# Optimization experiments

Hardware: AMD Instinct MI355X
Metric: run time of the kernel (lower is better)

## Reference

```python
import jax, jax.numpy as jnp
import numpy as np
import math

D_MODEL = 1024
N_HEADS = 16
RANK = 16
SCALE = 16.0
T_LEN = 2048
BSZ = 2


def setup_inputs() -> dict:
    key = jax.random.key(0)
    ks = jax.random.split(key, 12)
    d, r = D_MODEL, RANK
    inp = {
        "query": jax.random.normal(ks[0], (T_LEN, BSZ, d), dtype=jnp.float32),
        "key": jax.random.normal(ks[1], (T_LEN, BSZ, d), dtype=jnp.float32),
        "value": jax.random.normal(ks[2], (T_LEN, BSZ, d), dtype=jnp.float32),
        "need_weights": 0,
        "attn_mask": 0,
        "in_proj_weight": jax.random.normal(ks[3], (3 * d, d), dtype=jnp.float32) * 0.02,
        "in_proj_bias": jax.random.normal(ks[4], (3 * d,), dtype=jnp.float32) * 0.02,
        "out_w": jax.random.normal(ks[5], (d, d), dtype=jnp.float32) * 0.02,
        "out_b": jax.random.normal(ks[6], (d,), dtype=jnp.float32) * 0.02,
        "k_a": jax.random.normal(ks[7], (r, d), dtype=jnp.float32) * 0.02,
        "k_b": jax.random.normal(ks[8], (r, d), dtype=jnp.float32) * 0.02,
        "v_a": jax.random.normal(ks[9], (r, d), dtype=jnp.float32) * 0.02,
        "v_b": jax.random.normal(ks[10], (r, d), dtype=jnp.float32) * 0.02,
    }
    return inp


def reference(query, key, value, need_weights, attn_mask,
              in_proj_weight, in_proj_bias, out_w, out_b,
              k_a, k_b, v_a, v_b):
    # NOTE: original module computes q,k,v all from `query` (self-attention);
    # `key`, `value`, `need_weights`, `attn_mask` are unused in the math.
    T, B, d = query.shape
    H = N_HEADS
    hd = d // H
    qkv = query @ in_proj_weight.T + in_proj_bias  # (T, B, 3d)
    q, k, v = jnp.split(qkv, 3, axis=-1)
    s = SCALE / RANK
    # LoRA low-rank updates on K and V (computed from query)
    k = k + s * ((query @ k_a.T) @ k_b)
    v = v + s * ((query @ v_a.T) @ v_b)
    # split heads: (T, B, H, hd)
    qh = q.reshape(T, B, H, hd)
    kh = k.reshape(T, B, H, hd)
    vh = v.reshape(T, B, H, hd)
    scale = 1.0 / math.sqrt(hd)
    scores = jnp.einsum('tbhd,sbhd->bhts', qh * scale, kh)  # (B, H, T, T)
    attn = jax.nn.softmax(scores, axis=-1)
    out = jnp.einsum('bhts,sbhd->tbhd', attn, vh).reshape(T, B, d)
    out = out @ out_w.T + out_b
    return out
```

## Files before the change

kernel.cpp:

```cpp
#include <hip/hip_runtime.h>
#include <stdint.h>

#define DEVI __device__ __forceinline__

typedef unsigned short u16;
typedef __attribute__((ext_vector_type(4))) float f32x4;
typedef __attribute__((ext_vector_type(16))) float f32x16;
typedef __attribute__((ext_vector_type(8))) short bf16x8;
typedef __attribute__((ext_vector_type(2))) unsigned int u32x2;

constexpr int T_LEN = 2048;
constexpr int BSZ   = 2;
constexpr int DM    = 1024;
constexpr int NH    = 16;
constexpr int HD    = 64;
constexpr int MROWS = T_LEN * BSZ;
constexpr float LORA_S = 16.0f / 16.0f;
constexpr float QSCALE = 0.125f * 1.4426950408889634f;

DEVI u16 f2bf(float x) {
  union { float f; uint32_t u; } v; v.f = x;
  uint32_t r = (v.u + 0x7FFFu + ((v.u >> 16) & 1u)) >> 16;
  return (u16)r;
}

DEVI uint32_t pk2bf(float a, float b) {
  return (uint32_t)f2bf(a) | ((uint32_t)f2bf(b) << 16);
}

DEVI uint32_t e2r(float x) {
  union { float f; uint32_t u; } v;
  v.f = __builtin_amdgcn_exp2f(x);
  return v.u;
}

DEVI void gload_lds16(const void* g, void* l) {
  __builtin_amdgcn_global_load_lds(
      (const __attribute__((address_space(1))) void*)g,
      (__attribute__((address_space(3))) void*)l, 16, 0, 0);
}

DEVI f32x4 mfma16(bf16x8 a, bf16x8 b, f32x4 c) {
  return __builtin_amdgcn_mfma_f32_16x16x32_bf16(a, b, c, 0, 0, 0);
}
DEVI f32x16 mfma32(bf16x8 a, bf16x8 b, f32x16 c) {
  return __builtin_amdgcn_mfma_f32_32x32x16_bf16(a, b, c, 0, 0, 0);
}

DEVI int kvswz(int rc, int l) { return rc * 128 + ((l ^ (rc & 15)) << 3); }

#define WAITBAR(N)                                        \
  do {                                                    \
    asm volatile("s_waitcnt vmcnt(" #N ")" ::: "memory"); \
    __builtin_amdgcn_sched_barrier(0);                    \
    __builtin_amdgcn_s_barrier();                         \
    __builtin_amdgcn_sched_barrier(0);                    \
  } while (0)

#define BARO()                                            \
  do {                                                    \
    __builtin_amdgcn_sched_barrier(0);                    \
    __builtin_amdgcn_s_barrier();                         \
    __builtin_amdgcn_sched_barrier(0);                    \
  } while (0)

__global__ void prep_kernel(const float* __restrict__ query,
                            const float* __restrict__ W,
                            const float* __restrict__ ka, const float* __restrict__ kb,
                            const float* __restrict__ va, const float* __restrict__ vb,
                            const float* __restrict__ ow,
                            u16* __restrict__ Wm, u16* __restrict__ Wo,
                            u16* __restrict__ Aq) {
  const int W3 = 3 * DM * DM;
  const int WO = DM * DM;
  const int AQ = MROWS * DM;
  const int total = W3 + WO + AQ;
  for (int idx = blockIdx.x * blockDim.x + threadIdx.x; idx < total;
       idx += gridDim.x * blockDim.x) {
    if (idx < W3) {
      const int n = idx >> 10, k = idx & 1023;
      float w = W[idx];
      if (n >= 2 * DM) {
        const int n2 = n - 2 * DM;
        float a = 0.f;
#pragma unroll
        for (int r = 0; r < 16; ++r) a += va[r * DM + k] * vb[r * DM + n2];
        w += LORA_S * a;
      } else if (n >= DM) {
        const int n2 = n - DM;
        float a = 0.f;
#pragma unroll
        for (int r = 0; r < 16; ++r) a += ka[r * DM + k] * kb[r * DM + n2];
        w += LORA_S * a;
      }
      Wm[idx] = f2bf(w);
    } else if (idx < W3 + WO) {
      const int i = idx - W3;
      Wo[i] = f2bf(ow[i]);
    } else {
      const int i = idx - W3 - WO;
      Aq[i] = f2bf(query[i]);
    }
  }
}

template <int EPIL>
__global__ __launch_bounds__(256, 4) void gemm_bt(
    const u16* __restrict__ A, const u16* __restrict__ Bt,
    const float* __restrict__ bias, float* __restrict__ Cf,
    u16* __restrict__ Qb, u16* __restrict__ Kb, u16* __restrict__ Vt,
    int M, int N, int K) {
  constexpr int BM = 128, BN = 128, BK = 32;
  __shared__ alignas(16) u16 SM[2][2][4096];
  const int tid = threadIdx.x;
  const int wv = tid >> 6, ln = tid & 63;
  const int l16 = ln & 15, lhi = ln >> 4;

  const int bid = blockIdx.x;
  const int half = (N >> 7) >> 1;
  const int x = bid & 7, j = bid >> 3;
  const int rq = x >> 1, ch = x & 1;
  const int jc = j % half, jr = j / half;
  const int row0 = (rq * 8 + jr) * BM;
  const int col0 = (ch * half + jc) * BN;
  const int wr = (wv >> 1) * 64, wc = (wv & 1) * 64;

  f32x4 acc[4][4];
#pragma unroll
  for (int i = 0; i < 4; ++i)
#pragma unroll
    for (int j2 = 0; j2 < 4; ++j2) acc[i][j2] = f32x4{0.f, 0.f, 0.f, 0.f};

  const int lrA = wv * 16 + (ln >> 3);
  const int lrB = lrA + 8;
  const int s_ = ln & 7;
  const int la = s_ ^ (lrA & 7), lb = s_ ^ (lrB & 7);
  const int ra = lrA + 64 * (la >> 2), ca = (la & 3) * 8;
  const int rb = lrB + 64 * (lb >> 2), cb = (lb & 3) * 8;

  const u16* pa0 = A + (size_t)(row0 + ra) * K + ca;
  const u16* pa1 = A + (size_t)(row0 + rb) * K + cb;
  const u16* pb0 = Bt + (size_t)(col0 + ra) * K + ca;
  const u16* pb1 = Bt + (size_t)(col0 + rb) * K + cb;

  auto stagep = [&](int buf) {
    gload_lds16(pa0, &SM[buf][0][(wv * 16) * 64]);
    gload_lds16(pa1, &SM[buf][0][(wv * 16 + 8) * 64]);
    gload_lds16(pb0, &SM[buf][1][(wv * 16) * 64]);
    gload_lds16(pb1, &SM[buf][1][(wv * 16 + 8) * 64]);
    pa0 += BK; pa1 += BK; pb0 += BK; pb1 += BK;
  };

  auto compute = [&](int buf) {
    const u16* Al = SM[buf][0];
    const u16* Bl = SM[buf][1];
    bf16x8 af[4], bfr[4];
#pragma unroll
    for (int m = 0; m < 4; ++m) {
      const int r = wr + m * 16 + l16, lr = r & 63;
      const int sl = (lhi | ((r >> 6) << 2)) ^ (lr & 7);
      af[m] = *(const bf16x8*)&Al[lr * 64 + sl * 8];
    }
#pragma unroll
    for (int n = 0; n < 4; ++n) {
      const int r = wc + n * 16 + l16, lr = r & 63;
      const int sl = (lhi | ((r >> 6) << 2)) ^ (lr & 7);
      bfr[n] = *(const bf16x8*)&Bl[lr * 64 + sl * 8];
    }
#pragma unroll
    for (int m = 0; m < 4; ++m)
#pragma unroll
      for (int n = 0; n < 4; ++n) acc[m][n] = mfma16(af[m], bfr[n], acc[m][n]);
  };

  const int NS = K / BK;
  stagep(0); stagep(1);

  for (int t = 0; t < NS - 2; t += 2) {
    WAITBAR(4); compute(0); BARO(); stagep(0);
    WAITBAR(4); compute(1); BARO(); stagep(1);
  }
  WAITBAR(4); compute(0);
  WAITBAR(0); compute(1);

  if constexpr (EPIL == 0) {
    if (col0 >= 2 * DM) {
      u16* Cl = (u16*)SM;
      __syncthreads();
#pragma unroll
      for (int m = 0; m < 4; ++m)
#pragma unroll
        for (int n = 0; n < 4; ++n) {
          const int lc = wc + n * 16 + l16;
          const float bc = bias[col0 + lc];
#pragma unroll
          for (int r = 0; r < 4; ++r) {
            const int rl = wr + m * 16 + lhi * 4 + r;
            const int tl = rl >> 1, bb = rl & 1;
            Cl[lc * 128 + bb * 64 + (((tl >> 3) ^ (lc & 7)) << 3) + (tl & 7)] =
                f2bf(acc[m][n][r] + bc);
          }
        }
      __syncthreads();
      const int h0 = (col0 - 2 * DM) >> 6;
      const int t0 = row0 >> 1;
#pragma unroll
      for (int i = 0; i < 8; ++i) {
        const int cid = i * 256 + tid;
        const int lc = cid >> 4, bb = (cid >> 3) & 1, tc = cid & 7;
        bf16x8 ch2 = *(const bf16x8*)&Cl[lc * 128 + bb * 64 + ((tc ^ (lc & 7)) << 3)];
        const int h = h0 + (lc >> 6), dd = lc & 63;
        *(bf16x8*)&Vt[(((size_t)(bb * NH + h)) * HD + dd) * T_LEN + t0 + tc * 8] = ch2;
      }
      return;
    }
  }

#pragma unroll
  for (int m = 0; m < 4; ++m) {
#pragma unroll
    for (int n = 0; n < 4; ++n) {
      const int col = col0 + wc + n * 16 + l16;
      const float bc = bias[col];
#pragma unroll
      for (int r = 0; r < 4; ++r) {
        const int row = row0 + wr + m * 16 + lhi * 4 + r;
        const float v = acc[m][n][r] + bc;
        if constexpr (EPIL == 0) {
          const int t = row >> 1, b = row & 1;
          if (col < DM) {
            const int h = col >> 6, dd = col & 63;
            Qb[(((size_t)(b * NH + h)) * T_LEN + t) * HD + dd] = f2bf(v * QSCALE);
          } else {
            const int c2 = col - DM, h = c2 >> 6, dd = c2 & 63;
            Kb[(((size_t)(b * NH + h)) * T_LEN + t) * HD + dd] = f2bf(v);
          }
        } else {
          Cf[(size_t)row * N + col] = v;
        }
      }
    }
  }
}

__global__ __launch_bounds__(256) void attn_kernel(const u16* __restrict__ Qb,
                                                   const u16* __restrict__ Kb,
                                                   const u16* __restrict__ Vt,
                                                   u16* __restrict__ Ob) {
  constexpr int KBLK = 64;
  __shared__ alignas(16) u16 KV[4][2][32 * 128];

  const int tid = threadIdx.x;
  const int wv = tid >> 6, ln = tid & 63;
  const int l32 = ln & 31, hi = ln >> 5;

  const int bid = blockIdx.x;
  const int lb = (bid & 7) * 64 + (bid >> 3);
  const int bh = lb >> 4;
  const int b = bh >> 4, h = bh & 15;
  const int q0 = (lb & 15) * 128 + wv * 32;

  const u16* Qh = Qb + (size_t)bh * T_LEN * HD;
  const u16* Kh = Kb + (size_t)bh * T_LEN * HD;
  const u16* Vh = Vt + (size_t)bh * HD * T_LEN;

  bf16x8 qf[4];
#pragma unroll
  for (int kd = 0; kd < 4; ++kd)
    qf[kd] = *(const bf16x8*)&Qh[(size_t)(q0 + l32) * HD + kd * 16 + hi * 8];

  bf16x8 ones;
#pragma unroll
  for (int i = 0; i < 8; ++i) ones[i] = (short)0x3F80;

  f32x16 ot[2] = {f32x16{}, f32x16{}};
  f32x16 lacc = f32x16{};

  const int g_row = ln >> 4;
  const int g_s   = ln & 15;
  const int j0 = wv * 2, j1 = wv * 2 + 1;
  const int row0r = 4 * j0 + g_row, row1r = 4 * j1 + g_row;
  const int l0 = g_s ^ (row0r & 15), l1 = g_s ^ (row1r & 15);
  const int lr0 = row0r + 32 * (l0 >> 3), lr1 = row1r + 32 * (l1 >> 3);
  const int c80 = (l0 & 7) * 8, c81 = (l1 & 7) * 8;

  const u16* ks0 = Kh + (size_t)lr0 * HD + c80;
  const u16* ks1 = Kh + (size_t)lr1 * HD + c81;
  const u16* vs0 = Vh + (size_t)lr0 * T_LEN + c80;
  const u16* vs1 = Vh + (size_t)lr1 * T_LEN + c81;

  auto stagep = [&](int buf) {
    gload_lds16(ks0, &KV[buf][0][j0 * 512]);
    gload_lds16(ks1, &KV[buf][0][j1 * 512]);
    gload_lds16(vs0, &KV[buf][1][j0 * 512]);
    gload_lds16(vs1, &KV[buf][1][j1 * 512]);
    ks0 += KBLK * HD; ks1 += KBLK * HD; vs0 += KBLK; vs1 += KBLK;
  };

  auto compute = [&](int buf) {
    const u16* Kl = KV[buf][0];
    const u16* Vl = KV[buf][1];
    f32x16 st[2] = {f32x16{}, f32x16{}};
    __builtin_amdgcn_s_setprio(1);
#pragma unroll
    for (int kd = 0; kd < 4; ++kd) {
      bf16x8 k0 = *(const bf16x8*)&Kl[kvswz(l32, kd * 2 + hi)];
      bf16x8 k1 = *(const bf16x8*)&Kl[kvswz(l32, 8 + kd * 2 + hi)];
      st[0] = mfma32(k0, qf[kd], st[0]);
      st[1] = mfma32(k1, qf[kd], st[1]);
    }
    __builtin_amdgcn_s_setprio(0);
    uint32_t c[2][8];
#pragma unroll
    for (int mk = 0; mk < 2; ++mk)
#pragma unroll
      for (int d = 0; d < 8; ++d)
        c[mk][d] = __builtin_amdgcn_perm(e2r(st[mk][2 * d + 1]),
                                         e2r(st[mk][2 * d]), 0x07060302u);
    __builtin_amdgcn_s_setprio(1);
#pragma unroll
    for (int ksl = 0; ksl < 4; ++ksl) {
      const int mk = ksl >> 1, s2 = ksl & 1;
      uint32_t a0 = c[mk][4 * s2 + 0], b0 = c[mk][4 * s2 + 2];
      uint32_t a1 = c[mk][4 * s2 + 1], b1 = c[mk][4 * s2 + 3];
      u32x2 r0 = __builtin_amdgcn_permlane32_swap(a0, b0, false, false);
      u32x2 r1 = __builtin_amdgcn_permlane32_swap(a1, b1, false, false);
      union { bf16x8 v; uint32_t u[4]; } pu;
      pu.u[0] = r0[0]; pu.u[1] = r1[0]; pu.u[2] = r0[1]; pu.u[3] = r1[1];
      bf16x8 vf0 = *(const bf16x8*)&Vl[kvswz(l32, ksl * 2 + hi)];
      bf16x8 vf1 = *(const bf16x8*)&Vl[kvswz(l32, 8 + ksl * 2 + hi)];
      ot[0] = mfma32(vf0, pu.v, ot[0]);
      ot[1] = mfma32(vf1, pu.v, ot[1]);
      lacc = mfma32(ones, pu.v, lacc);
    }
    __builtin_amdgcn_s_setprio(0);
  };

  stagep(0); stagep(1); stagep(2); stagep(3);

  for (int it7 = 0; it7 < 7; ++it7) {
    WAITBAR(8); compute(0); compute(1); BARO(); stagep(0); stagep(1);
    WAITBAR(8); compute(2); compute(3); BARO(); stagep(2); stagep(3);
  }
  WAITBAR(8); compute(0); compute(1);
  WAITBAR(0); compute(2); compute(3);

  const float inv = 1.0f / lacc[0];
  const size_t rowbase = ((size_t)(q0 + l32) * BSZ + b) * DM + h * HD;
#pragma unroll
  for (int dt = 0; dt < 2; ++dt) {
#pragma unroll
    for (int g = 0; g < 4; ++g) {
      const float v0 = ot[dt][4 * g + 0] * inv;
      const float v1 = ot[dt][4 * g + 1] * inv;
      const float v2 = ot[dt][4 * g + 2] * inv;
      const float v3 = ot[dt][4 * g + 3] * inv;
      u32x2 w; w[0] = pk2bf(v0, v1); w[1] = pk2bf(v2, v3);
      const int dim = dt * 32 + 8 * g + 4 * hi;
      *(u32x2*)&Ob[rowbase + dim] = w;
    }
  }
}

extern "C" void kernel_launch(void* const* d_in, const int* in_sizes, int n_in,
                              void* d_out, int out_size, void* d_ws, size_t ws_size,
                              hipStream_t stream) {
  const float* query = (const float*)d_in[0];
  const float* W     = (const float*)d_in[5];
  const float* bias  = (const float*)d_in[6];
  const float* ow    = (const float*)d_in[7];
  const float* ob    = (const float*)d_in[8];
  const float* ka    = (const float*)d_in[9];
  const float* kb    = (const float*)d_in[10];
  const float* va    = (const float*)d_in[11];
  const float* vb    = (const float*)d_in[12];

  char* ws = (char*)d_ws;
  u16* Wm = (u16*)ws; ws += (size_t)3 * DM * DM * 2;
  u16* Wo = (u16*)ws; ws += (size_t)DM * DM * 2;
  u16* Aq = (u16*)ws; ws += (size_t)MROWS * DM * 2;
  u16* Qb = (u16*)ws; ws += (size_t)BSZ * NH * T_LEN * HD * 2;
  u16* Kb = (u16*)ws; ws += (size_t)BSZ * NH * T_LEN * HD * 2;
  u16* Vt = (u16*)ws; ws += (size_t)BSZ * NH * T_LEN * HD * 2;
  u16* Ob = (u16*)ws; ws += (size_t)MROWS * DM * 2;

  prep_kernel<<<2048, 256, 0, stream>>>(query, W, ka, kb, va, vb, ow, Wm, Wo, Aq);

  gemm_bt<0><<<(MROWS / 128) * ((3 * DM) / 128), 256, 0, stream>>>(
      Aq, Wm, bias, nullptr, Qb, Kb, Vt, MROWS, 3 * DM, DM);

  attn_kernel<<<512, 256, 0, stream>>>(Qb, Kb, Vt, Ob);

  gemm_bt<1><<<(MROWS / 128) * (DM / 128), 256, 0, stream>>>(
      Ob, Wo, ob, (float*)d_out, nullptr, nullptr, nullptr, MROWS, DM, DM);
}
```

Before: 117.4 us.

## Split attention KV range in two across blocks and merge partials

Each attention block now covers only half of the key/value sequence, which doubles the grid to 1024 blocks. The shared-memory ring shrinks from four stages to two, and launch bounds request four blocks per CU to raise occupancy. Unnormalized fp32 partial outputs and row sums go to workspace, and a new merge kernel adds the two halves, normalizes and writes bf16. This depends on the softmax having no running max (the exp2 form is presumably unnormalized), and it costs an extra launch plus fp32 partial traffic.

```diff
diff --git a/kernel.cpp b/kernel.cpp
--- a/kernel.cpp
+++ b/kernel.cpp
@@ -243,22 +243,23 @@
   }
 }
 
-__global__ __launch_bounds__(256) void attn_kernel(const u16* __restrict__ Qb,
-                                                   const u16* __restrict__ Kb,
-                                                   const u16* __restrict__ Vt,
-                                                   u16* __restrict__ Ob) {
+__global__ __launch_bounds__(256, 4) void attn_kernel(
+    const u16* __restrict__ Qb, const u16* __restrict__ Kb,
+    const u16* __restrict__ Vt, float* __restrict__ Opart,
+    float* __restrict__ Lpart) {
   constexpr int KBLK = 64;
-  __shared__ alignas(16) u16 KV[4][2][32 * 128];
+  __shared__ alignas(16) u16 KV[2][2][32 * 128];
 
   const int tid = threadIdx.x;
   const int wv = tid >> 6, ln = tid & 63;
   const int l32 = ln & 31, hi = ln >> 5;
 
   const int bid = blockIdx.x;
-  const int lb = (bid & 7) * 64 + (bid >> 3);
-  const int bh = lb >> 4;
-  const int b = bh >> 4, h = bh & 15;
-  const int q0 = (lb & 15) * 128 + wv * 32;
+  const int lb = (bid & 7) * 128 + (bid >> 3);
+  const int bh = lb >> 5;
+  const int rem = lb & 31;
+  const int kvh = rem >> 4;
+  const int q0 = (rem & 15) * 128 + wv * 32;
 
   const u16* Qh = Qb + (size_t)bh * T_LEN * HD;
   const u16* Kh = Kb + (size_t)bh * T_LEN * HD;
@@ -284,10 +285,11 @@
   const int lr0 = row0r + 32 * (l0 >> 3), lr1 = row1r + 32 * (l1 >> 3);
   const int c80 = (l0 & 7) * 8, c81 = (l1 & 7) * 8;
 
-  const u16* ks0 = Kh + (size_t)lr0 * HD + c80;
-  const u16* ks1 = Kh + (size_t)lr1 * HD + c81;
-  const u16* vs0 = Vh + (size_t)lr0 * T_LEN + c80;
-  const u16* vs1 = Vh + (size_t)lr1 * T_LEN + c81;
+  const int kt0 = kvh * (T_LEN / 2);
+  const u16* ks0 = Kh + (size_t)(kt0 + lr0) * HD + c80;
+  const u16* ks1 = Kh + (size_t)(kt0 + lr1) * HD + c81;
+  const u16* vs0 = Vh + (size_t)lr0 * T_LEN + kt0 + c80;
+  const u16* vs1 = Vh + (size_t)lr1 * T_LEN + kt0 + c81;
 
   auto stagep = [&](int buf) {
     gload_lds16(ks0, &KV[buf][0][j0 * 512]);
@@ -336,29 +338,49 @@
     __builtin_amdgcn_s_setprio(0);
   };
 
-  stagep(0); stagep(1); stagep(2); stagep(3);
-
-  for (int it7 = 0; it7 < 7; ++it7) {
-    WAITBAR(8); compute(0); compute(1); BARO(); stagep(0); stagep(1);
-    WAITBAR(8); compute(2); compute(3); BARO(); stagep(2); stagep(3);
-  }
-  WAITBAR(8); compute(0); compute(1);
-  WAITBAR(0); compute(2); compute(3);
-
-  const float inv = 1.0f / lacc[0];
-  const size_t rowbase = ((size_t)(q0 + l32) * BSZ + b) * DM + h * HD;
+  stagep(0); stagep(1);
+  for (int it = 0; it < 7; ++it) {
+    WAITBAR(4); compute(0); BARO(); stagep(0);
+    WAITBAR(4); compute(1); BARO(); stagep(1);
+  }
+  WAITBAR(4); compute(0);
+  WAITBAR(0); compute(1);
+
+  const int q = q0 + l32;
+  const size_t obase = ((size_t)(kvh * 32 + bh) * T_LEN + q) * HD;
 #pragma unroll
   for (int dt = 0; dt < 2; ++dt) {
 #pragma unroll
     for (int g = 0; g < 4; ++g) {
-      const float v0 = ot[dt][4 * g + 0] * inv;
-      const float v1 = ot[dt][4 * g + 1] * inv;
-      const float v2 = ot[dt][4 * g + 2] * inv;
-      const float v3 = ot[dt][4 * g + 3] * inv;
-      u32x2 w; w[0] = pk2bf(v0, v1); w[1] = pk2bf(v2, v3);
-      const int dim = dt * 32 + 8 * g + 4 * hi;
-      *(u32x2*)&Ob[rowbase + dim] = w;
-    }
+      f32x4 w;
+      w[0] = ot[dt][4 * g + 0]; w[1] = ot[dt][4 * g + 1];
+      w[2] = ot[dt][4 * g + 2]; w[3] = ot[dt][4 * g + 3];
+      *(f32x4*)&Opart[obase + dt * 32 + 8 * g + 4 * hi] = w;
+    }
+  }
+  if (hi == 0) Lpart[(size_t)(kvh * 32 + bh) * T_LEN + q] = lacc[0];
+}
+
+__global__ __launch_bounds__(256) void merge_kernel(
+    const float* __restrict__ Op, const float* __restrict__ Lp,
+    u16* __restrict__ Ob) {
+  constexpr int HALF_O = 32 * T_LEN * HD;
+  constexpr int HALF_L = 32 * T_LEN;
+  const int total = HALF_O / 4;
+  for (int i = blockIdx.x * blockDim.x + threadIdx.x; i < total;
+       i += gridDim.x * blockDim.x) {
+    const int d4 = (i & 15) * 4;
+    const int q  = (i >> 4) & (T_LEN - 1);
+    const int bh = i >> 15;
+    const size_t base = ((size_t)bh * T_LEN + q) * HD + d4;
+    f32x4 a = *(const f32x4*)&Op[base];
+    f32x4 c = *(const f32x4*)&Op[base + HALF_O];
+    const float inv = 1.0f / (Lp[bh * T_LEN + q] + Lp[bh * T_LEN + q + HALF_L]);
+    u32x2 w;
+    w[0] = pk2bf((a[0] + c[0]) * inv, (a[1] + c[1]) * inv);
+    w[1] = pk2bf((a[2] + c[2]) * inv, (a[3] + c[3]) * inv);
+    const int b = bh >> 4, h = bh & 15;
+    *(u32x2*)&Ob[((size_t)q * BSZ + b) * DM + h * HD + d4] = w;
   }
 }
 
@@ -383,13 +405,17 @@
   u16* Kb = (u16*)ws; ws += (size_t)BSZ * NH * T_LEN * HD * 2;
   u16* Vt = (u16*)ws; ws += (size_t)BSZ * NH * T_LEN * HD * 2;
   u16* Ob = (u16*)ws; ws += (size_t)MROWS * DM * 2;
+  float* Opart = (float*)ws; ws += (size_t)2 * 32 * T_LEN * HD * 4;
+  float* Lpart = (float*)ws; ws += (size_t)2 * 32 * T_LEN * 4;
 
   prep_kernel<<<2048, 256, 0, stream>>>(query, W, ka, kb, va, vb, ow, Wm, Wo, Aq);
 
   gemm_bt<0><<<(MROWS / 128) * ((3 * DM) / 128), 256, 0, stream>>>(
       Aq, Wm, bias, nullptr, Qb, Kb, Vt, MROWS, 3 * DM, DM);
 
-  attn_kernel<<<512, 256, 0, stream>>>(Qb, Kb, Vt, Ob);
+  attn_kernel<<<1024, 256, 0, stream>>>(Qb, Kb, Vt, Opart, Lpart);
+
+  merge_kernel<<<2048, 256, 0, stream>>>(Opart, Lpart, Ob);
 
   gemm_bt<1><<<(MROWS / 128) * (DM / 128), 256, 0, stream>>>(
       Ob, Wo, ob, (float*)d_out, nullptr, nullptr, nullptr, MROWS, DM, DM);
```

Result: slower. 157.6 us (+34.2%).
